# Kernel tuning notes

Hardware: AMD Instinct MI355X
Metric: run time of the kernel (lower is better)

## Reference

```python
import jax, jax.numpy as jnp
import numpy as np

B, S, E, H = 4, 1024, 256, 12  # batch, seq, emb_dim, num_heads; per-head dim == E (module quirk)


def setup_inputs() -> dict:
    key = jax.random.key(0)
    ks = jax.random.split(key, 9)
    s = 0.02
    x = jax.random.normal(ks[0], (B, S, E), dtype=jnp.float32)
    # additive causal mask (the module's tril buffer is unused; mask arrives via attention_mask)
    causal = jnp.tril(jnp.ones((S, S), dtype=jnp.float32))
    attention_mask = ((1.0 - causal) * -10000.0)[None, None, :, :]
    Wq = jax.random.normal(ks[1], (E, E * H), dtype=jnp.float32) * s
    bq = jnp.zeros((E * H,), dtype=jnp.float32)
    Wk = jax.random.normal(ks[2], (E, E * H), dtype=jnp.float32) * s
    bk = jnp.zeros((E * H,), dtype=jnp.float32)
    Wv = jax.random.normal(ks[3], (E, E * H), dtype=jnp.float32) * s
    bv = jnp.zeros((E * H,), dtype=jnp.float32)
    Wfc = jax.random.normal(ks[4], (E * H, E), dtype=jnp.float32) * s
    bfc = jnp.zeros((E,), dtype=jnp.float32)
    return {"x": x, "attention_mask": attention_mask, "Wq": Wq, "bq": bq,
            "Wk": Wk, "bk": bk, "Wv": Wv, "bv": bv, "Wfc": Wfc, "bfc": bfc}


def _split_heads(t):
    # (B, S, H*E) -> (B, H, S, E)
    b, s, _ = t.shape
    return t.reshape(b, s, H, E).transpose(0, 2, 1, 3)


def reference(x, attention_mask, Wq, bq, Wk, bk, Wv, bv, Wfc, bfc):
    q = _split_heads(x @ Wq + bq)
    k = _split_heads(x @ Wk + bk)
    v = _split_heads(x @ Wv + bv)
    scale = 1.0 / jnp.sqrt(jnp.asarray(E, dtype=x.dtype))
    scores = jnp.einsum('bhqd,bhkd->bhqk', q, k) * scale + attention_mask
    probs = jax.nn.softmax(scores, axis=-1)  # dropout p=0 in eval reference
    ctx = jnp.einsum('bhqk,bhkd->bhqd', probs, v)
    merged = ctx.transpose(0, 2, 1, 3).reshape(x.shape[0], x.shape[1], H * E)
    return merged @ Wfc + bfc
```

## Files before the change

### kernel.cpp

```cpp
#include <hip/hip_runtime.h>

#define BATCH 4
#define SEQ   1024
#define EMB   256
#define NH    12
#define EH    3072
#define MROWS 4096

typedef __attribute__((ext_vector_type(8))) short bf16x8;
typedef __attribute__((ext_vector_type(4))) float f32x4;
typedef __attribute__((ext_vector_type(4))) short short4v;

__device__ __forceinline__ short f2bf(float f) {
  union { float f; unsigned u; } x; x.f = f;
  unsigned r = x.u + 0x7fffu + ((x.u >> 16) & 1u);
  return (short)(r >> 16);
}

__device__ __forceinline__ void gload_lds16(const void* g, void* l) {
  __builtin_amdgcn_global_load_lds(
      (const __attribute__((address_space(1))) unsigned*)g,
      (__attribute__((address_space(3))) unsigned*)l, 16, 0, 0);
}

__global__ __launch_bounds__(256) void cast_x_kernel(const float* __restrict__ in,
                                                     short* __restrict__ out) {
  int i = (blockIdx.x * 256 + threadIdx.x) * 4;
  float4 v = *(const float4*)(in + i);
  short4v o;
  o[0] = f2bf(v.x); o[1] = f2bf(v.y); o[2] = f2bf(v.z); o[3] = f2bf(v.w);
  *(short4v*)(out + i) = o;
}

__global__ __launch_bounds__(256) void transpose_qkv_kernel(const float* __restrict__ Wq,
                                                            const float* __restrict__ Wk,
                                                            const float* __restrict__ Wv,
                                                            short* __restrict__ Wt) {
  __shared__ float tile[32][33];
  const float* W = blockIdx.z == 0 ? Wq : (blockIdx.z == 1 ? Wk : Wv);
  short* o = Wt + (size_t)blockIdx.z * EH * EMB;
  const int n0 = blockIdx.x * 32, k0 = blockIdx.y * 32;
  const int tx = threadIdx.x & 31, ty = threadIdx.x >> 5;
#pragma unroll
  for (int i = 0; i < 4; i++)
    tile[ty + 8 * i][tx] = W[(size_t)(k0 + ty + 8 * i) * EH + n0 + tx];
  __syncthreads();
#pragma unroll
  for (int i = 0; i < 4; i++) {
    int nr = ty + 8 * i;
    o[(size_t)(n0 + nr) * EMB + k0 + tx] = f2bf(tile[tx][nr]);
  }
}

__global__ __launch_bounds__(256) void transpose_cast_kernel(const float* __restrict__ W,
                                                             short* __restrict__ Wt,
                                                             int K, int N) {
  __shared__ float tile[32][33];
  const int n0 = blockIdx.x * 32, k0 = blockIdx.y * 32;
  const int tx = threadIdx.x & 31, ty = threadIdx.x >> 5;
#pragma unroll
  for (int i = 0; i < 4; i++)
    tile[ty + 8 * i][tx] = W[(size_t)(k0 + ty + 8 * i) * N + n0 + tx];
  __syncthreads();
#pragma unroll
  for (int i = 0; i < 4; i++) {
    int nr = ty + 8 * i;
    Wt[(size_t)(n0 + nr) * K + k0 + tx] = f2bf(tile[tx][nr]);
  }
}

__global__ __launch_bounds__(256) void qkv_gemm_kernel(const short* __restrict__ A,
                                                       const short* __restrict__ Bt,
                                                       const float* __restrict__ bq,
                                                       const float* __restrict__ bk,
                                                       const float* __restrict__ bv,
                                                       short* __restrict__ qout,
                                                       short* __restrict__ kout,
                                                       short* __restrict__ vout) {
  constexpr int BM = 128, BN = 128, BK = 32, K = EMB;
  __shared__ short As[2][BM * BK];
  __shared__ short Bs[2][BN * BK];
  const int tid = threadIdx.x;
  const int w = tid >> 6, lane = tid & 63;
  const int wm = w >> 1, wn = w & 1;
  const int l15 = lane & 15, l4 = lane >> 4;
  const int m0 = blockIdx.x * BM, n0 = blockIdx.y * BN;

  f32x4 acc[4][4] = {};

  int srow[2], scol[2];
#pragma unroll
  for (int i = 0; i < 2; i++) {
    const int idx = i * 256 + tid;
    const int rp = idx >> 3, sp = idx & 7, sl = sp ^ (rp & 7);
    srow[i] = rp * 2 + (sl >> 2);
    scol[i] = (sl & 3) * 8;
  }

#define QKV_STAGE(bu, k0)                                                        \
  {                                                                              \
    _Pragma("unroll") for (int i = 0; i < 2; i++) {                              \
      const int idx = i * 256 + tid;                                             \
      gload_lds16(A + (size_t)(m0 + srow[i]) * K + (k0) + scol[i],               \
                  (char*)&As[bu][0] + idx * 16);                                 \
      gload_lds16(Bt + (size_t)(n0 + srow[i]) * K + (k0) + scol[i],              \
                  (char*)&Bs[bu][0] + idx * 16);                                 \
    }                                                                            \
  }

  QKV_STAGE(0, 0);
  asm volatile("s_waitcnt vmcnt(0)" ::: "memory");
  __syncthreads();

  int bu = 0;
  for (int k0 = 0; k0 < K; k0 += BK) {
    if (k0 + BK < K) QKV_STAGE(bu ^ 1, k0 + BK);

    bf16x8 af[4], bfr[4];
    const int sp = ((l15 & 1) * 4 + l4) ^ (l15 >> 1);
#pragma unroll
    for (int mt = 0; mt < 4; mt++)
      af[mt] = *(const bf16x8*)&As[bu][(wm * 32 + mt * 8 + (l15 >> 1)) * 64 + sp * 8];
#pragma unroll
    for (int nt = 0; nt < 4; nt++)
      bfr[nt] = *(const bf16x8*)&Bs[bu][(wn * 32 + nt * 8 + (l15 >> 1)) * 64 + sp * 8];
    __builtin_amdgcn_s_setprio(1);
#pragma unroll
    for (int mt = 0; mt < 4; mt++)
#pragma unroll
      for (int nt = 0; nt < 4; nt++)
        acc[mt][nt] = __builtin_amdgcn_mfma_f32_16x16x32_bf16(af[mt], bfr[nt], acc[mt][nt], 0, 0, 0);
    __builtin_amdgcn_s_setprio(0);

    asm volatile("s_waitcnt vmcnt(0)" ::: "memory");
    __syncthreads();
    bu ^= 1;
  }

  const int region = n0 / 3072;
  const float* bias = region == 0 ? bq : (region == 1 ? bk : bv);
  const float kQScale = 0.09016844f;
#pragma unroll
  for (int nt = 0; nt < 4; nt++) {
    const int n = n0 + wn * 64 + nt * 16 + l15;
    const int col = n - region * 3072;
    const float bvv = bias[col];
#pragma unroll
    for (int mt = 0; mt < 4; mt++) {
      const int mrow = m0 + wm * 64 + mt * 16 + 4 * l4;
      f32x4 v = acc[mt][nt];
      if (region == 0) {
#pragma unroll
        for (int r = 0; r < 4; r++)
          qout[(size_t)(mrow + r) * EH + col] = f2bf((v[r] + bvv) * kQScale);
      } else if (region == 1) {
#pragma unroll
        for (int r = 0; r < 4; r++)
          kout[(size_t)(mrow + r) * EH + col] = f2bf(v[r] + bvv);
      } else {
        const int bb = mrow >> 10;
        const int s  = mrow & 1023;
        const int h  = col >> 8, d = col & 255;
        short4v o4;
        o4[0] = f2bf(v[0] + bvv); o4[1] = f2bf(v[1] + bvv);
        o4[2] = f2bf(v[2] + bvv); o4[3] = f2bf(v[3] + bvv);
        *(short4v*)&vout[((size_t)(bb * NH + h) * EMB + d) * SEQ + s] = o4;
      }
    }
  }
#undef QKV_STAGE
}

__global__ __launch_bounds__(256) void fc_gemm_kernel(const short* __restrict__ A,
                                                      const short* __restrict__ Bt,
                                                      const float* __restrict__ bias,
                                                      float* __restrict__ Cout,
                                                      int M, int N, int K) {
  constexpr int BM = 64, BN = 64, BK = 64;
  __shared__ short As[2][BM * BK];
  __shared__ short Bs[2][BN * BK];
  const int tid = threadIdx.x;
  const int w = tid >> 6, lane = tid & 63;
  const int wm = w >> 1, wn = w & 1;
  const int l15 = lane & 15, l4 = lane >> 4;
  const int m0 = blockIdx.x * BM, n0 = blockIdx.y * BN;

  f32x4 acc[2][2] = {};

  int srow[2], scol[2];
#pragma unroll
  for (int i = 0; i < 2; i++) {
    const int idx = i * 256 + tid;
    const int row = idx >> 3, sp = idx & 7, sl = sp ^ (row & 7);
    srow[i] = row;
    scol[i] = sl * 8;
  }

#define FC_STAGE(bu, k0)                                                         \
  {                                                                              \
    _Pragma("unroll") for (int i = 0; i < 2; i++) {                              \
      const int idx = i * 256 + tid;                                             \
      gload_lds16(A + (size_t)(m0 + srow[i]) * K + (k0) + scol[i],               \
                  (char*)&As[bu][0] + idx * 16);                                 \
      gload_lds16(Bt + (size_t)(n0 + srow[i]) * K + (k0) + scol[i],              \
                  (char*)&Bs[bu][0] + idx * 16);                                 \
    }                                                                            \
  }

  FC_STAGE(0, 0);
  asm volatile("s_waitcnt vmcnt(0)" ::: "memory");
  __syncthreads();

  int bu = 0;
  for (int k0 = 0; k0 < K; k0 += BK) {
    if (k0 + BK < K) FC_STAGE(bu ^ 1, k0 + BK);

    bf16x8 af[2][2], bfr[2][2];
#pragma unroll
    for (int kst = 0; kst < 2; kst++) {
      const int sp = (kst * 4 + l4) ^ (l15 & 7);
#pragma unroll
      for (int mt = 0; mt < 2; mt++)
        af[mt][kst] = *(const bf16x8*)&As[bu][(wm * 32 + mt * 16 + l15) * 64 + sp * 8];
#pragma unroll
      for (int nt = 0; nt < 2; nt++)
        bfr[nt][kst] = *(const bf16x8*)&Bs[bu][(wn * 32 + nt * 16 + l15) * 64 + sp * 8];
    }
    __builtin_amdgcn_s_setprio(1);
#pragma unroll
    for (int kst = 0; kst < 2; kst++)
#pragma unroll
      for (int mt = 0; mt < 2; mt++)
#pragma unroll
        for (int nt = 0; nt < 2; nt++)
          acc[mt][nt] = __builtin_amdgcn_mfma_f32_16x16x32_bf16(af[mt][kst], bfr[nt][kst], acc[mt][nt], 0, 0, 0);
    __builtin_amdgcn_s_setprio(0);

    asm volatile("s_waitcnt vmcnt(0)" ::: "memory");
    __syncthreads();
    bu ^= 1;
  }

#pragma unroll
  for (int nt = 0; nt < 2; nt++) {
    const int n = n0 + wn * 32 + nt * 16 + l15;
    const float bvv = bias[n];
#pragma unroll
    for (int mt = 0; mt < 2; mt++) {
      const int mrow = m0 + wm * 32 + mt * 16 + 4 * l4;
      f32x4 v = acc[mt][nt];
#pragma unroll
      for (int r = 0; r < 4; r++)
        Cout[(size_t)(mrow + r) * N + n] = v[r] + bvv;
    }
  }
#undef FC_STAGE
}

__global__ __launch_bounds__(512) void attn_kernel(const short* __restrict__ Q,
                                                   const short* __restrict__ Kg,
                                                   const short* __restrict__ Vt,
                                                   short* __restrict__ Ctx) {
  __shared__ short Ks[2][8192];
  __shared__ short Vs[2][8192];
  __shared__ short Ps[8][512];
  const int tid = threadIdx.x, w = tid >> 6, lane = tid & 63;
  const int l15 = lane & 15, l4 = lane >> 4;
  const int bh = blockIdx.x, b = bh / NH, h = bh % NH;
  const int qt = (gridDim.y - 1) - blockIdx.y;
  const int q0 = qt * 128;
  const int qw0 = q0 + w * 16;
  const int ntiles = 4 * qt + 4;

  const float kMaskL2 = -14426.95f;
  const float kThrL2  = 11.5f;

  const short* Kbase = Kg + (size_t)b * SEQ * EH + h * EMB;
  const short* Vbase = Vt + (size_t)bh * EMB * SEQ;

  int koff[2], voff[2];
#pragma unroll
  for (int i = 0; i < 2; i++) {
    const int idx = i * 512 + tid;
    {
      const int kv = (idx >> 3) & 31, sp = idx & 7, sl = sp ^ (kv & 7);
      koff[i] = kv * EH + (idx >> 8) * 64 + sl * 8;
    }
    {
      const int dp = idx >> 3, sp = idx & 7, sl = sp ^ (dp & 7);
      voff[i] = (dp * 2 + (sl >> 2)) * SEQ + (sl & 3) * 8;
    }
  }

  bf16x8 qf[8];
  {
    const short* qp = Q + (size_t)(b * SEQ + qw0 + l15) * EH + h * EMB + 8 * l4;
#pragma unroll
    for (int kst = 0; kst < 8; kst++) qf[kst] = *(const bf16x8*)(qp + 32 * kst);
  }

#pragma unroll
  for (int i = 0; i < 2; i++) {
    const int idx = i * 512 + tid;
    gload_lds16(Kbase + koff[i], (char*)&Ks[0][0] + idx * 16);
    gload_lds16(Vbase + voff[i], (char*)&Vs[0][0] + idx * 16);
  }
  asm volatile("s_waitcnt vmcnt(0)" ::: "memory");
  __syncthreads();

  f32x4 o[16] = {};
  float mst = -1e30f, lst = 0.f;

  int bu = 0;
  for (int t = 0; t < ntiles; t++) {
    const int kv0 = t * 32;

    if (t + 1 < ntiles) {
      const short* kp = Kbase + (size_t)(kv0 + 32) * EH;
      const short* vp = Vbase + kv0 + 32;
#pragma unroll
      for (int i = 0; i < 2; i++) {
        const int idx = i * 512 + tid;
        gload_lds16(kp + koff[i], (char*)&Ks[bu ^ 1][0] + idx * 16);
        gload_lds16(vp + voff[i], (char*)&Vs[bu ^ 1][0] + idx * 16);
      }
    }

    if (kv0 <= qw0 + 15) {
      f32x4 sf[2] = {};
      __builtin_amdgcn_s_setprio(1);
#pragma unroll
      for (int nt = 0; nt < 2; nt++)
#pragma unroll
        for (int kst = 0; kst < 8; kst++) {
          const int sp = (((kst & 1) << 2) + l4) ^ (l15 & 7);
          bf16x8 kf = *(const bf16x8*)&Ks[bu][(kst >> 1) * 2048 + (nt * 16 + l15) * 64 + sp * 8];
          sf[nt] = __builtin_amdgcn_mfma_f32_16x16x32_bf16(kf, qf[kst], sf[nt], 0, 0, 0);
        }
      __builtin_amdgcn_s_setprio(0);

      const bool maskt = (kv0 + 31 > qw0);
      float sval[2][4];
      float mxl = -1e30f;
#pragma unroll
      for (int nt = 0; nt < 2; nt++)
#pragma unroll
        for (int r = 0; r < 4; r++) {
          float s = sf[nt][r];
          if (maskt) {
            const int kv = kv0 + nt * 16 + 4 * l4 + r;
            s += (kv > qw0 + l15) ? kMaskL2 : 0.0f;
          }
          sval[nt][r] = s;
          mxl = fmaxf(mxl, s);
        }
      float mx = fmaxf(mxl, __shfl_xor(mxl, 16));
      mx = fmaxf(mx, __shfl_xor(mx, 32));
      const bool skipt = __all(mx <= mst + kThrL2);
      float mref, fsc;
      if (skipt) {
        fsc = 1.0f;
        mref = mst;
      } else {
        float mnew = fmaxf(mst, mx);
        fsc = exp2f(mst - mnew);
        mst = mnew;
        mref = mnew;
      }
      float pp[2][4];
      float lsum = 0.f;
#pragma unroll
      for (int nt = 0; nt < 2; nt++)
#pragma unroll
        for (int r = 0; r < 4; r++) {
          float e = exp2f(sval[nt][r] - mref);
          pp[nt][r] = e;
          lsum += e;
        }
      lst = lst * fsc + lsum;

      if (!skipt) {
        float fv[4];
#pragma unroll
        for (int r = 0; r < 4; r++)
          fv[r] = __shfl(fsc, (lane & 48) + 4 * (lane >> 4) + r);
#pragma unroll
        for (int nt = 0; nt < 16; nt++) {
          o[nt][0] *= fv[0]; o[nt][1] *= fv[1];
          o[nt][2] *= fv[2]; o[nt][3] *= fv[3];
        }
      }

#pragma unroll
      for (int nt = 0; nt < 2; nt++)
#pragma unroll
        for (int r = 0; r < 4; r++) {
          const int col  = nt * 16 + 4 * l4 + r;
          const int pseg = (col >> 3) ^ ((l15 >> 1) & 3);
          Ps[w][l15 * 32 + pseg * 8 + (col & 7)] = f2bf(pp[nt][r]);
        }

      const int aseg = l4 ^ ((l15 >> 1) & 3);
      bf16x8 af = *(const bf16x8*)&Ps[w][l15 * 32 + aseg * 8];
      const int vsp = ((l15 & 1) * 4 + l4) ^ (l15 >> 1);
      __builtin_amdgcn_s_setprio(1);
#pragma unroll
      for (int nt = 0; nt < 16; nt++) {
        const int dp = nt * 8 + (l15 >> 1);
        bf16x8 vf = *(const bf16x8*)&Vs[bu][dp * 64 + vsp * 8];
        o[nt] = __builtin_amdgcn_mfma_f32_16x16x32_bf16(af, vf, o[nt], 0, 0, 0);
      }
      __builtin_amdgcn_s_setprio(0);
    }

    asm volatile("s_waitcnt vmcnt(0)" ::: "memory");
    __syncthreads();
    bu ^= 1;
  }

  lst += __shfl_xor(lst, 16);
  lst += __shfl_xor(lst, 32);
  const float inv = 1.f / lst;
  float invv[4];
#pragma unroll
  for (int r = 0; r < 4; r++)
    invv[r] = __shfl(inv, (lane & 48) + 4 * (lane >> 4) + r);

  const int mrow = b * SEQ + qw0 + 4 * l4;
#pragma unroll
  for (int nt = 0; nt < 16; nt++) {
    const int d = h * EMB + nt * 16 + l15;
#pragma unroll
    for (int r = 0; r < 4; r++)
      Ctx[(size_t)(mrow + r) * EH + d] = f2bf(o[nt][r] * invv[r]);
  }
}

extern "C" void kernel_launch(void* const* d_in, const int* in_sizes, int n_in,
                              void* d_out, int out_size, void* d_ws, size_t ws_size,
                              hipStream_t stream) {
  const float* x   = (const float*)d_in[0];
  const float* Wq  = (const float*)d_in[2];
  const float* bq  = (const float*)d_in[3];
  const float* Wk  = (const float*)d_in[4];
  const float* bk  = (const float*)d_in[5];
  const float* Wv  = (const float*)d_in[6];
  const float* bv  = (const float*)d_in[7];
  const float* Wfc = (const float*)d_in[8];
  const float* bfc = (const float*)d_in[9];
  float* out = (float*)d_out;

  short* ws    = (short*)d_ws;
  short* xb    = ws;
  short* wqkvt = xb + 1048576;
  short* wfct  = wqkvt + 3 * 786432;
  short* q     = wfct + 786432;
  short* k     = q + 12582912;
  short* vt    = k + 12582912;
  short* ctx   = vt + 12582912;

  cast_x_kernel<<<1024, 256, 0, stream>>>(x, xb);
  transpose_qkv_kernel<<<dim3(EH / 32, EMB / 32, 3), 256, 0, stream>>>(Wq, Wk, Wv, wqkvt);
  transpose_cast_kernel<<<dim3(EMB / 32, EH / 32), 256, 0, stream>>>(Wfc, wfct, EH, EMB);

  qkv_gemm_kernel<<<dim3(MROWS / 128, 9216 / 128), 256, 0, stream>>>(
      xb, wqkvt, bq, bk, bv, q, k, vt);

  attn_kernel<<<dim3(BATCH * NH, SEQ / 128), 512, 0, stream>>>(q, k, vt, ctx);

  fc_gemm_kernel<<<dim3(MROWS / 64, EMB / 64), 256, 0, stream>>>(ctx, wfct, bfc, out, MROWS, EMB, EH);
}
```

Baseline: 160.4 us.

## Deepen K tiles in QKV and FC GEMMs and pack truncated P stores

The QKV GEMM now stages BK=64 per iteration with a plain row-major swizzled LDS layout and 16-row fragments. The FC GEMM stages BK=128 with a 16-way swizzle. Both halve the number of K iterations and their barrier/waitcnt syncs. Separately, the attention kernel packs the probability values into bf16 by truncation and writes them as one 8-byte LDS store instead of four rounded 2-byte stores. This cuts ALU and LDS store work but changes rounding to truncation, and the larger tiles raise LDS use, which may lower occupancy.

```diff
diff --git a/kernel.cpp b/kernel.cpp
--- a/kernel.cpp
+++ b/kernel.cpp
@@ -15,6 +15,12 @@
   union { float f; unsigned u; } x; x.f = f;
   unsigned r = x.u + 0x7fffu + ((x.u >> 16) & 1u);
   return (short)(r >> 16);
+}
+
+__device__ __forceinline__ unsigned pack_trunc(float a, float b) {
+  union { float f; unsigned u; } x, y;
+  x.f = a; y.f = b;
+  return (x.u >> 16) | (y.u & 0xffff0000u);
 }
 
 __device__ __forceinline__ void gload_lds16(const void* g, void* l) {
@@ -77,29 +83,29 @@
                                                        short* __restrict__ qout,
                                                        short* __restrict__ kout,
                                                        short* __restrict__ vout) {
-  constexpr int BM = 128, BN = 128, BK = 32, K = EMB;
+  constexpr int BM = 128, BK = 64, K = EMB;
   __shared__ short As[2][BM * BK];
-  __shared__ short Bs[2][BN * BK];
+  __shared__ short Bs[2][BM * BK];
   const int tid = threadIdx.x;
   const int w = tid >> 6, lane = tid & 63;
   const int wm = w >> 1, wn = w & 1;
   const int l15 = lane & 15, l4 = lane >> 4;
-  const int m0 = blockIdx.x * BM, n0 = blockIdx.y * BN;
+  const int m0 = blockIdx.x * BM, n0 = blockIdx.y * BM;
 
   f32x4 acc[4][4] = {};
 
-  int srow[2], scol[2];
-#pragma unroll
-  for (int i = 0; i < 2; i++) {
+  int srow[4], scol[4];
+#pragma unroll
+  for (int i = 0; i < 4; i++) {
     const int idx = i * 256 + tid;
-    const int rp = idx >> 3, sp = idx & 7, sl = sp ^ (rp & 7);
-    srow[i] = rp * 2 + (sl >> 2);
-    scol[i] = (sl & 3) * 8;
+    const int row = idx >> 3, sp = idx & 7, sl = sp ^ (row & 7);
+    srow[i] = row;
+    scol[i] = sl * 8;
   }
 
 #define QKV_STAGE(bu, k0)                                                        \
   {                                                                              \
-    _Pragma("unroll") for (int i = 0; i < 2; i++) {                              \
+    _Pragma("unroll") for (int i = 0; i < 4; i++) {                              \
       const int idx = i * 256 + tid;                                             \
       gload_lds16(A + (size_t)(m0 + srow[i]) * K + (k0) + scol[i],               \
                   (char*)&As[bu][0] + idx * 16);                                 \
@@ -116,21 +122,24 @@
   for (int k0 = 0; k0 < K; k0 += BK) {
     if (k0 + BK < K) QKV_STAGE(bu ^ 1, k0 + BK);
 
-    bf16x8 af[4], bfr[4];
-    const int sp = ((l15 & 1) * 4 + l4) ^ (l15 >> 1);
-#pragma unroll
-    for (int mt = 0; mt < 4; mt++)
-      af[mt] = *(const bf16x8*)&As[bu][(wm * 32 + mt * 8 + (l15 >> 1)) * 64 + sp * 8];
-#pragma unroll
-    for (int nt = 0; nt < 4; nt++)
-      bfr[nt] = *(const bf16x8*)&Bs[bu][(wn * 32 + nt * 8 + (l15 >> 1)) * 64 + sp * 8];
-    __builtin_amdgcn_s_setprio(1);
-#pragma unroll
-    for (int mt = 0; mt < 4; mt++)
+#pragma unroll
+    for (int kst = 0; kst < 2; kst++) {
+      const int sp = (kst * 4 + l4) ^ (l15 & 7);
+      bf16x8 af[4], bfr[4];
+#pragma unroll
+      for (int mt = 0; mt < 4; mt++)
+        af[mt] = *(const bf16x8*)&As[bu][(wm * 64 + mt * 16 + l15) * 64 + sp * 8];
 #pragma unroll
       for (int nt = 0; nt < 4; nt++)
-        acc[mt][nt] = __builtin_amdgcn_mfma_f32_16x16x32_bf16(af[mt], bfr[nt], acc[mt][nt], 0, 0, 0);
-    __builtin_amdgcn_s_setprio(0);
+        bfr[nt] = *(const bf16x8*)&Bs[bu][(wn * 64 + nt * 16 + l15) * 64 + sp * 8];
+      __builtin_amdgcn_s_setprio(1);
+#pragma unroll
+      for (int mt = 0; mt < 4; mt++)
+#pragma unroll
+        for (int nt = 0; nt < 4; nt++)
+          acc[mt][nt] = __builtin_amdgcn_mfma_f32_16x16x32_bf16(af[mt], bfr[nt], acc[mt][nt], 0, 0, 0);
+      __builtin_amdgcn_s_setprio(0);
+    }
 
     asm volatile("s_waitcnt vmcnt(0)" ::: "memory");
     __syncthreads();
@@ -176,29 +185,29 @@
                                                       const float* __restrict__ bias,
                                                       float* __restrict__ Cout,
                                                       int M, int N, int K) {
-  constexpr int BM = 64, BN = 64, BK = 64;
+  constexpr int BM = 64, BK = 128;
   __shared__ short As[2][BM * BK];
-  __shared__ short Bs[2][BN * BK];
+  __shared__ short Bs[2][BM * BK];
   const int tid = threadIdx.x;
   const int w = tid >> 6, lane = tid & 63;
   const int wm = w >> 1, wn = w & 1;
   const int l15 = lane & 15, l4 = lane >> 4;
-  const int m0 = blockIdx.x * BM, n0 = blockIdx.y * BN;
+  const int m0 = blockIdx.x * BM, n0 = blockIdx.y * BM;
 
   f32x4 acc[2][2] = {};
 
-  int srow[2], scol[2];
-#pragma unroll
-  for (int i = 0; i < 2; i++) {
+  int srow[4], scol[4];
+#pragma unroll
+  for (int i = 0; i < 4; i++) {
     const int idx = i * 256 + tid;
-    const int row = idx >> 3, sp = idx & 7, sl = sp ^ (row & 7);
+    const int row = idx >> 4, sp = idx & 15, sl = sp ^ (row & 15);
     srow[i] = row;
     scol[i] = sl * 8;
   }
 
 #define FC_STAGE(bu, k0)                                                         \
   {                                                                              \
-    _Pragma("unroll") for (int i = 0; i < 2; i++) {                              \
+    _Pragma("unroll") for (int i = 0; i < 4; i++) {                              \
       const int idx = i * 256 + tid;                                             \
       gload_lds16(A + (size_t)(m0 + srow[i]) * K + (k0) + scol[i],               \
                   (char*)&As[bu][0] + idx * 16);                                 \
@@ -215,26 +224,24 @@
   for (int k0 = 0; k0 < K; k0 += BK) {
     if (k0 + BK < K) FC_STAGE(bu ^ 1, k0 + BK);
 
-    bf16x8 af[2][2], bfr[2][2];
-#pragma unroll
-    for (int kst = 0; kst < 2; kst++) {
-      const int sp = (kst * 4 + l4) ^ (l15 & 7);
+#pragma unroll
+    for (int kst = 0; kst < 4; kst++) {
+      const int sp = (kst * 4 + l4) ^ l15;
+      bf16x8 af[2], bfr[2];
 #pragma unroll
       for (int mt = 0; mt < 2; mt++)
-        af[mt][kst] = *(const bf16x8*)&As[bu][(wm * 32 + mt * 16 + l15) * 64 + sp * 8];
+        af[mt] = *(const bf16x8*)&As[bu][(wm * 32 + mt * 16 + l15) * 128 + sp * 8];
 #pragma unroll
       for (int nt = 0; nt < 2; nt++)
-        bfr[nt][kst] = *(const bf16x8*)&Bs[bu][(wn * 32 + nt * 16 + l15) * 64 + sp * 8];
-    }
-    __builtin_amdgcn_s_setprio(1);
-#pragma unroll
-    for (int kst = 0; kst < 2; kst++)
+        bfr[nt] = *(const bf16x8*)&Bs[bu][(wn * 32 + nt * 16 + l15) * 128 + sp * 8];
+      __builtin_amdgcn_s_setprio(1);
 #pragma unroll
       for (int mt = 0; mt < 2; mt++)
 #pragma unroll
         for (int nt = 0; nt < 2; nt++)
-          acc[mt][nt] = __builtin_amdgcn_mfma_f32_16x16x32_bf16(af[mt][kst], bfr[nt][kst], acc[mt][nt], 0, 0, 0);
-    __builtin_amdgcn_s_setprio(0);
+          acc[mt][nt] = __builtin_amdgcn_mfma_f32_16x16x32_bf16(af[mt], bfr[nt], acc[mt][nt], 0, 0, 0);
+      __builtin_amdgcn_s_setprio(0);
+    }
 
     asm volatile("s_waitcnt vmcnt(0)" ::: "memory");
     __syncthreads();
@@ -392,13 +399,14 @@
       }
 
 #pragma unroll
-      for (int nt = 0; nt < 2; nt++)
-#pragma unroll
-        for (int r = 0; r < 4; r++) {
-          const int col  = nt * 16 + 4 * l4 + r;
-          const int pseg = (col >> 3) ^ ((l15 >> 1) & 3);
-          Ps[w][l15 * 32 + pseg * 8 + (col & 7)] = f2bf(pp[nt][r]);
-        }
+      for (int nt = 0; nt < 2; nt++) {
+        uint2 pk;
+        pk.x = pack_trunc(pp[nt][0], pp[nt][1]);
+        pk.y = pack_trunc(pp[nt][2], pp[nt][3]);
+        const int col0 = nt * 16 + 4 * l4;
+        const int pseg = (col0 >> 3) ^ ((l15 >> 1) & 3);
+        *(uint2*)&Ps[w][l15 * 32 + pseg * 8 + (col0 & 7)] = pk;
+      }
 
       const int aseg = l4 ^ ((l15 >> 1) & 3);
       bf16x8 af = *(const bf16x8*)&Ps[w][l15 * 32 + aseg * 8];
```

After: 151.0 us. 5.8% less time.
